# Kernel tuning notes

Measured on AMD Instinct MI355X. Metric: run time of the kernel, lower is better.

## Reference

```python
import jax, jax.numpy as jnp
import numpy as np
import math

B, S, HID = 2, 2048, 1024
NH = 16
HD = HID // NH          # 64
VD = HD // 2            # 32 value dim
TD = HD - VD            # 32 type dim
EPS = 1e-6


def setup_inputs() -> dict:
    key = jax.random.key(0)
    ks = jax.random.split(key, 12)
    std = 1.0 / math.sqrt(HID)
    xav = math.sqrt(6.0 / (TD + TD))
    return {
        "x": jax.random.normal(ks[0], (B, S, HID), dtype=jnp.float32),
        "q_w": jax.random.uniform(ks[1], (HID, HID), jnp.float32, -std, std),
        "q_b": jax.random.uniform(ks[2], (HID,), jnp.float32, -std, std),
        "k_w": jax.random.uniform(ks[3], (HID, HID), jnp.float32, -std, std),
        "k_b": jax.random.uniform(ks[4], (HID,), jnp.float32, -std, std),
        "v_w": jax.random.uniform(ks[5], (HID, HID), jnp.float32, -std, std),
        "v_b": jax.random.uniform(ks[6], (HID,), jnp.float32, -std, std),
        "out_w": jax.random.uniform(ks[7], (HID, HID), jnp.float32, -std, std),
        "out_b": jax.random.uniform(ks[8], (HID,), jnp.float32, -std, std),
        "type_bilinear": jax.random.uniform(ks[9], (NH, TD, TD), jnp.float32, -xav, xav),
        "type_bias": jnp.full((NH,), 2.0, dtype=jnp.float32),
        "mask": jnp.ones((B, S), dtype=jnp.int32),
    }


def reference(x, q_w, q_b, k_w, k_b, v_w, v_b, out_w, out_b, type_bilinear, type_bias, mask):
    # projections: [B,S,HID] -> [B,NH,S,HD]
    def proj(w, b):
        y = jnp.einsum("bsi,io->bso", x, w) + b
        return y.reshape(B, S, NH, HD).transpose(0, 2, 1, 3)

    q = proj(q_w, q_b)
    k = proj(k_w, k_b)
    v = proj(v_w, v_b)

    q_val, q_type = q[..., :VD], q[..., VD:]
    k_val, k_type = k[..., :VD], k[..., VD:]

    # standard value score: [B,NH,S,S]
    val_scores = jnp.einsum("bhqd,bhkd->bhqk", q_val, k_val) / math.sqrt(VD)

    # per-head bilinear type score: q_type @ W_h @ k_type^T + bias_h
    qt = jnp.einsum("bhqd,hde->bhqe", q_type, type_bilinear)
    type_scores = jnp.einsum("bhqe,bhke->bhqk", qt, k_type) + type_bias[None, :, None, None]
    type_unif = jax.nn.sigmoid(type_scores)

    scores = val_scores + jnp.log(type_unif + EPS)

    # mask: [B,S] -> broadcast over heads and query dim (keys masked)
    m = (mask[:, None, None, :] != 0)
    scores = jnp.where(m, scores, -jnp.inf)

    attn = jax.nn.softmax(scores, axis=-1)
    out = jnp.einsum("bhqk,bhkd->bhqd", attn, v)          # [B,NH,S,HD]
    out = out.transpose(0, 2, 1, 3).reshape(B, S, HID)
    return jnp.einsum("bsi,io->bso", out, out_w) + out_b
```

## Files before the change

kernel.cpp:

```cpp
#include <hip/hip_runtime.h>
#include <hip/hip_bf16.h>
#include <math.h>

typedef __attribute__((ext_vector_type(8))) short bf16x8;
typedef __attribute__((ext_vector_type(4))) short bf16x4;
typedef __attribute__((ext_vector_type(4))) float f32x4;
typedef __attribute__((ext_vector_type(4))) int   i32x4;

#define NHh 16
#define Sq  2048
#define HIDq 1024
#define HDq 64
#define LOG2E 1.4426950408889634f

#if __has_builtin(__builtin_amdgcn_exp2f)
#define EXP2F(x) __builtin_amdgcn_exp2f(x)
#else
#define EXP2F(x) exp2f(x)
#endif
#if __has_builtin(__builtin_amdgcn_rcpf)
#define RCPF(x) __builtin_amdgcn_rcpf(x)
#else
#define RCPF(x) (1.0f/(x))
#endif

#if __has_builtin(__builtin_amdgcn_mfma_f32_16x16x16bf16_1k)
__device__ __forceinline__ f32x4 MFMA16(bf16x4 a, bf16x4 b, f32x4 c){
  return __builtin_amdgcn_mfma_f32_16x16x16bf16_1k(a, b, c, 0, 0, 0);
}
#else
__device__ __forceinline__ f32x4 MFMA16(bf16x4 a, bf16x4 b, f32x4 c){
  asm volatile("v_mfma_f32_16x16x16_bf16 %0, %1, %2, %0\n\ts_nop 7\n\ts_nop 7"
               : "+v"(c) : "v"(a), "v"(b));
  return c;
}
#endif

__device__ __forceinline__ unsigned short f2bf(float f){
  union { float f; unsigned u; } v; v.f = f;
  unsigned r = v.u + 0x7fffu + ((v.u >> 16) & 1u);
  return (unsigned short)(r >> 16);
}
__device__ __forceinline__ float bf2f(unsigned short s){
  union { unsigned u; float f; } v; v.u = ((unsigned)s) << 16;
  return v.f;
}
__device__ __forceinline__ unsigned pk2bf(float lo, float hi){
  union { __hip_bfloat162 h; unsigned u; } w;
  w.h = __float22bfloat162_rn(make_float2(lo, hi));
  return w.u;
}

__device__ __forceinline__ void gload_lds16(const unsigned short* g, unsigned short* l){
  __builtin_amdgcn_global_load_lds(
      (const __attribute__((address_space(1))) unsigned int*)g,
      (__attribute__((address_space(3))) unsigned int*)l, 16, 0, 0);
}

__global__ __launch_bounds__(256) void convert_x(const float* __restrict__ in,
                                                 unsigned short* __restrict__ out, int n8,
                                                 const int* __restrict__ mask,
                                                 unsigned short* __restrict__ Mbf){
  int bid = blockIdx.x;
  int nmain = gridDim.x - 2;
  if (bid >= nmain){
    int base = (bid - nmain)*2048 + threadIdx.x*8;
    #pragma unroll
    for (int j=0;j<8;j++) Mbf[base+j] = mask[base+j] ? (unsigned short)0x3F80 : (unsigned short)0;
    return;
  }
  int i = bid*256 + threadIdx.x;
  if (i >= n8) return;
  const f32x4* p = (const f32x4*)(in + (size_t)i*8);
  f32x4 a = p[0], b = p[1];
  union { unsigned short us[8]; i32x4 v; } o;
  #pragma unroll
  for (int j=0;j<4;j++){ o.us[j] = f2bf(a[j]); o.us[4+j] = f2bf(b[j]); }
  *(i32x4*)(out + (size_t)i*8) = o.v;
}

__global__ __launch_bounds__(256) void transpose_w(const float* __restrict__ w0, const float* __restrict__ w1,
                                                   const float* __restrict__ w2, const float* __restrict__ w3,
                                                   unsigned short* __restrict__ wT){
  __shared__ float tile[32][33];
  int z = blockIdx.z;
  const float* w = (z==0)?w0:(z==1)?w1:(z==2)?w2:w3;
  unsigned short* dst = wT + (size_t)z*HIDq*HIDq;
  int tx = threadIdx.x, ty = threadIdx.y;
  int n0 = blockIdx.x*32, k0 = blockIdx.y*32;
  #pragma unroll
  for (int i=ty;i<32;i+=8) tile[i][tx] = w[(size_t)(k0+i)*HIDq + n0+tx];
  __syncthreads();
  #pragma unroll
  for (int i=ty;i<32;i+=8) dst[(size_t)(n0+i)*HIDq + k0+tx] = f2bf(tile[tx][i]);
}

__device__ __forceinline__ void gemm_core_gl(const unsigned short* __restrict__ Ag,
                                             const unsigned short* __restrict__ Bg,
                                             unsigned short* As, unsigned short* Bs,
                                             int t, int wv, int lane, int wr, int wc, int lr, int g,
                                             f32x4 acc[4][4]){
  for (int k0=0; k0<HIDq; k0+=64){
    __syncthreads();
    #pragma unroll
    for (int j=0;j<4;j++){
      int flat = (j*4+wv)*64 + lane;
      int row = flat>>3, c = flat&7;
      int srcc = (c ^ (row&7))*8;
      gload_lds16(Ag + (size_t)row*HIDq + k0 + srcc, &As[flat*8]);
      gload_lds16(Bg + (size_t)row*HIDq + k0 + srcc, &Bs[flat*8]);
    }
    __syncthreads();
    #pragma unroll
    for (int ks=0; ks<2; ks++){
      bf16x8 af[4], bfv[4];
      #pragma unroll
      for (int m=0;m<4;m++){
        int rr = wr + m*16 + lr;
        af[m]  = *(bf16x8*)&As[rr*64 + (((ks*4+g) ^ (rr&7))*8)];
      }
      #pragma unroll
      for (int n=0;n<4;n++){
        int rr = wc + n*16 + lr;
        bfv[n] = *(bf16x8*)&Bs[rr*64 + (((ks*4+g) ^ (rr&7))*8)];
      }
      #pragma unroll
      for (int n=0;n<4;n++)
        #pragma unroll
        for (int m=0;m<4;m++)
          acc[n][m] = __builtin_amdgcn_mfma_f32_16x16x32_bf16(bfv[n], af[m], acc[n][m], 0,0,0);
    }
  }
}

__global__ __launch_bounds__(256) void gemm_qkv(const unsigned short* __restrict__ xbf,
    const unsigned short* __restrict__ wT,
    const float* __restrict__ q_b, const float* __restrict__ k_b, const float* __restrict__ v_b,
    const int* __restrict__ mask,
    unsigned short* __restrict__ Qeff, unsigned short* __restrict__ Keff,
    unsigned short* __restrict__ Vt){
  __shared__ unsigned short As[128*64];
  __shared__ unsigned short Bs[128*64];
  const int t = threadIdx.x;
  const int wv = t>>6, lane = t&63, g = lane>>4, lr = lane&15;
  const int wr = (wv>>1)*64, wc = (wv&1)*64;
  f32x4 acc[4][4] = {};
  const int xb = blockIdx.x, yb = blockIdx.y;
  const float VS = 0.25501335f;

  if (xb < 16){
    const int row0 = yb*128, col0 = xb*128;
    gemm_core_gl(xbf + (size_t)row0*HIDq, wT + (size_t)col0*HIDq, As, Bs, t, wv, lane, wr, wc, lr, g, acc);
    #pragma unroll
    for (int n=0;n<4;n++){
      #pragma unroll
      for (int m=0;m<4;m++){
        int row = row0 + wr + m*16 + lr;
        int b_ = row>>11, ss = row&2047;
        int colb = col0 + wc + n*16 + g*4;
        int seg = colb>>10, cw = colb&1023;
        int hh = cw>>6, d = cw&63;
        const float* bp = seg ? k_b : q_b;
        f32x4 bb = *(const f32x4*)&bp[cw];
        float sc = seg ? 1.0f : (d < 32 ? VS : -LOG2E);
        unsigned short* E = seg ? Keff : Qeff;
        float v0 = (acc[n][m][0]+bb[0])*sc, v1 = (acc[n][m][1]+bb[1])*sc;
        float v2 = (acc[n][m][2]+bb[2])*sc, v3 = (acc[n][m][3]+bb[3])*sc;
        union { unsigned u[2]; unsigned long long ll; } W;
        W.u[0] = pk2bf(v0,v1); W.u[1] = pk2bf(v2,v3);
        *(unsigned long long*)&E[(((size_t)b_*NHh+hh)*Sq+ss)*HDq + d] = W.ll;
      }
    }
  } else {
    const int row0 = (xb-16)*128, col0 = yb*128;
    gemm_core_gl(wT + (size_t)2*HIDq*HIDq + (size_t)row0*HIDq, xbf + (size_t)col0*HIDq,
                 As, Bs, t, wv, lane, wr, wc, lr, g, acc);
    #pragma unroll
    for (int n=0;n<4;n++){
      #pragma unroll
      for (int m=0;m<4;m++){
        int chan = row0 + wr + m*16 + lr;
        int hh = chan>>6, d = chan&63;
        float bv = v_b[chan];
        int colb = col0 + wc + n*16 + g*4;
        int b_ = colb>>11, ss = colb&2047;
        i32x4 mk = *(const i32x4*)&mask[(size_t)b_*Sq + ss];
        float m0 = mk[0]?1.f:0.f, m1 = mk[1]?1.f:0.f, m2 = mk[2]?1.f:0.f, m3 = mk[3]?1.f:0.f;
        union { unsigned u[2]; unsigned long long ll; } W;
        W.u[0] = pk2bf((acc[n][m][0]+bv)*m0, (acc[n][m][1]+bv)*m1);
        W.u[1] = pk2bf((acc[n][m][2]+bv)*m2, (acc[n][m][3]+bv)*m3);
        *(unsigned long long*)&Vt[(((size_t)b_*NHh+hh)*HDq + d)*Sq + ss] = W.ll;
      }
    }
  }
}

__global__ __launch_bounds__(256) void gemm_out(const unsigned short* __restrict__ A,
                                                const unsigned short* __restrict__ Bt,
                                                const float* __restrict__ bias,
                                                float* __restrict__ C){
  __shared__ unsigned short As[128*64];
  __shared__ unsigned short Bs[64*64];
  const int t = threadIdx.x;
  const int wv = t>>6, lane = t&63, g = lane>>4, lr = lane&15;
  const int wr = (wv>>1)*64, wc = (wv&1)*32;
  const int row0 = blockIdx.y*128, col0 = blockIdx.x*64;
  f32x4 acc[2][4] = {};
  for (int k0=0; k0<HIDq; k0+=64){
    __syncthreads();
    #pragma unroll
    for (int j=0;j<4;j++){
      int flat = t + j*256;
      int row = flat>>3, c = flat&7;
      int srcc = (c ^ (row&7))*8;
      gload_lds16(A + (size_t)(row0+row)*HIDq + k0 + srcc, &As[flat*8]);
    }
    #pragma unroll
    for (int j=0;j<2;j++){
      int flat = t + j*256;
      int row = flat>>3, c = flat&7;
      int srcc = (c ^ (row&7))*8;
      gload_lds16(Bt + (size_t)(col0+row)*HIDq + k0 + srcc, &Bs[flat*8]);
    }
    __syncthreads();
    #pragma unroll
    for (int ks=0; ks<2; ks++){
      bf16x8 af[4], bfv[2];
      #pragma unroll
      for (int m=0;m<4;m++){
        int rr = wr + m*16 + lr;
        af[m]  = *(bf16x8*)&As[rr*64 + (((ks*4+g) ^ (rr&7))*8)];
      }
      #pragma unroll
      for (int n=0;n<2;n++){
        int rr = wc + n*16 + lr;
        bfv[n] = *(bf16x8*)&Bs[rr*64 + (((ks*4+g) ^ (rr&7))*8)];
      }
      #pragma unroll
      for (int n=0;n<2;n++)
        #pragma unroll
        for (int m=0;m<4;m++)
          acc[n][m] = __builtin_amdgcn_mfma_f32_16x16x32_bf16(bfv[n], af[m], acc[n][m], 0,0,0);
    }
  }
  #pragma unroll
  for (int n=0;n<2;n++){
    #pragma unroll
    for (int m=0;m<4;m++){
      int row = row0 + wr + m*16 + lr;
      int colb = col0 + wc + n*16 + g*4;
      f32x4 bb = *(const f32x4*)&bias[colb];
      f32x4 o = acc[n][m] + bb;
      *(f32x4*)&C[(size_t)row*HIDq + colb] = o;
    }
  }
}

__global__ __launch_bounds__(256,4) void attn_kernel(
    const unsigned short* __restrict__ Qe, const unsigned short* __restrict__ Ke,
    const unsigned short* __restrict__ Vt, const float* __restrict__ Tb,
    const float* __restrict__ tbias, const unsigned short* __restrict__ Mbf,
    unsigned short* __restrict__ Obuf)
{
  __shared__ __align__(16) unsigned char smem[40960];
  unsigned short* Kb0 = (unsigned short*)smem;
  unsigned short* Kb1 = (unsigned short*)(smem + 8192);
  unsigned short* Kb2 = (unsigned short*)(smem + 16384);
  unsigned short* Vb0 = (unsigned short*)(smem + 24576);
  unsigned short* Vb1 = (unsigned short*)(smem + 32768);
  float* qls = (float*)smem;
  unsigned short* qtls = Vb1;

  const int t = threadIdx.x;
  const int dd = blockIdx.x;
  const int slot = dd>>3, xcd = dd&7;
  const int x = slot & 31;
  const int bh = ((slot>>5)<<3) | xcd;
  const int h = bh & 15, b = bh >> 4;
  const int q0 = x*64;
  const int wv = t>>6, lane = t&63, g = lane>>4, lr = lane&15;

  const unsigned short* Qb  = Qe + (((size_t)b*NHh+h)*Sq + q0)*HDq;
  const unsigned short* Kb  = Ke + ((size_t)b*NHh+h)*(size_t)Sq*HDq;
  const unsigned short* Vtb = Vt + ((size_t)b*NHh+h)*(size_t)HDq*Sq;
  const unsigned short* Mbfb = Mbf + (size_t)b*Sq;

  {
    int row = t>>2, c8 = (t&3)*8;
    bf16x8 v = *(const bf16x8*)(Qb + (size_t)row*HDq + 32 + c8);
    #pragma unroll
    for (int j=0;j<8;j++) qls[row*33 + c8 + j] = bf2f((unsigned short)v[j]);
  }
  __syncthreads();
  {
    int row = t&63, e0 = (t>>6)*8;
    const float* Th = Tb + (size_t)h*1024;
    float a[8] = {};
    #pragma unroll 4
    for (int d=0; d<32; d++){
      float qd = qls[row*33 + d];
      const f32x4* tp = (const f32x4*)(Th + d*32 + e0);
      f32x4 t0 = tp[0], t1 = tp[1];
      a[0]+=qd*t0[0]; a[1]+=qd*t0[1]; a[2]+=qd*t0[2]; a[3]+=qd*t0[3];
      a[4]+=qd*t1[0]; a[5]+=qd*t1[1]; a[6]+=qd*t1[2]; a[7]+=qd*t1[3];
    }
    __syncthreads();
    union { unsigned u[2]; unsigned long long ll; } W0, W1;
    W0.u[0]=pk2bf(a[0],a[1]); W0.u[1]=pk2bf(a[2],a[3]);
    W1.u[0]=pk2bf(a[4],a[5]); W1.u[1]=pk2bf(a[6],a[7]);
    *(unsigned long long*)&qtls[row*40 + e0]     = W0.ll;
    *(unsigned long long*)&qtls[row*40 + e0 + 4] = W1.ll;
  }
  bf16x8 qvf = *(const bf16x8*)(Qb + (size_t)(wv*16+lr)*HDq + g*8);
  __syncthreads();
  bf16x8 qtn = *(const bf16x8*)&qtls[(wv*16+lr)*40 + g*8];
  __syncthreads();

  #pragma unroll
  for (int i=0;i<2;i++){
    int c = t + i*256;
    int kr = c>>3, kc = c&7;
    gload_lds16(Kb + (size_t)kr*HDq + ((kc ^ (kr&7))*8), Kb0 + c*8);
    int vd = c>>3, vc = c&7;
    gload_lds16(Vtb + (size_t)vd*Sq + ((vc ^ (vd&7))*8), Vb0 + c*8);
    gload_lds16(Kb + (size_t)(64+kr)*HDq + ((kc ^ (kr&7))*8), Kb1 + c*8);
  }
  __syncthreads();

  const float tbn = -tbias[h]*LOG2E;
  const f32x4 tbc = {tbn,tbn,tbn,tbn};
  const f32x4 zf = {0.f,0.f,0.f,0.f};
  f32x4 oT[4] = {};
  f32x4 lsum = {0.f,0.f,0.f,0.f};

  auto phase = [&](const unsigned short* Kc, const unsigned short* Vc, int key0,
                   bool stK, int keyK, unsigned short* Kn,
                   bool stV, int keyV, unsigned short* Vn, bool vm8){
    if (stK){
      #pragma unroll
      for (int i=0;i<2;i++){
        int c = t + i*256;
        int kr = c>>3, kc = c&7;
        gload_lds16(Kb + (size_t)(keyK+kr)*HDq + ((kc ^ (kr&7))*8), Kn + c*8);
      }
    }
    if (stV){
      #pragma unroll
      for (int i=0;i<2;i++){
        int c = t + i*256;
        int vd = c>>3, vc = c&7;
        gload_lds16(Vtb + (size_t)vd*Sq + keyV + ((vc ^ (vd&7))*8), Vn + c*8);
      }
    }
    if (vm8) asm volatile("s_waitcnt vmcnt(8)" ::: "memory");
    else     asm volatile("s_waitcnt vmcnt(4)" ::: "memory");
    __builtin_amdgcn_sched_barrier(0);
    __builtin_amdgcn_s_barrier();

    f32x4 sv[4], st[4];
    __builtin_amdgcn_s_setprio(1);
    #pragma unroll
    for (int ks=0; ks<4; ks++){
      const unsigned short* kb = Kc + (ks*16+lr)*64;
      bf16x8 kf0 = *(const bf16x8*)(kb + (((g  ) ^ (lr&7))*8));
      bf16x8 kf1 = *(const bf16x8*)(kb + (((4+g) ^ (lr&7))*8));
      sv[ks] = __builtin_amdgcn_mfma_f32_16x16x32_bf16(kf0, qvf, zf, 0,0,0);
      st[ks] = __builtin_amdgcn_mfma_f32_16x16x32_bf16(kf1, qtn, tbc, 0,0,0);
    }
    __builtin_amdgcn_s_setprio(0);
    bf16x4 pa[4];
    #pragma unroll
    for (int ks=0; ks<4; ks++){
      float p0 = EXP2F(sv[ks][0]) * RCPF(1.f + EXP2F(st[ks][0]));
      float p1 = EXP2F(sv[ks][1]) * RCPF(1.f + EXP2F(st[ks][1]));
      float p2 = EXP2F(sv[ks][2]) * RCPF(1.f + EXP2F(st[ks][2]));
      float p3 = EXP2F(sv[ks][3]) * RCPF(1.f + EXP2F(st[ks][3]));
      union { unsigned u[2]; bf16x4 v; } P_;
      P_.u[0] = pk2bf(p0,p1); P_.u[1] = pk2bf(p2,p3);
      pa[ks] = P_.v;
    }
    #pragma unroll
    for (int ks=0; ks<4; ks++){
      bf16x4 mfr = *(const bf16x4*)(Mbfb + key0 + ks*16 + g*4);
      __builtin_amdgcn_s_setprio(1);
      lsum = MFMA16(pa[ks], mfr, lsum);
      #pragma unroll
      for (int db=0; db<4; db++){
        bf16x4 vf = *(const bf16x4*)(Vc + (db*16+lr)*64 + (((2*ks + (g>>1)) ^ (lr&7))*8 + 4*(g&1)));
        oT[db] = MFMA16(pa[ks], vf, oT[db]);
      }
      __builtin_amdgcn_s_setprio(0);
    }
    __builtin_amdgcn_s_barrier();
  };

  for (int j=0; j<5; j++){
    int kt = j*384;
    phase(Kb0, Vb0, kt,      true, kt+128, Kb2,  true, kt+64,  Vb1, true);
    phase(Kb1, Vb1, kt+64,   true, kt+192, Kb0,  true, kt+128, Vb0, true);
    phase(Kb2, Vb0, kt+128,  true, kt+256, Kb1,  true, kt+192, Vb1, true);
    phase(Kb0, Vb1, kt+192,  true, kt+320, Kb2,  true, kt+256, Vb0, true);
    phase(Kb1, Vb0, kt+256,  true, kt+384, Kb0,  true, kt+320, Vb1, true);
    phase(Kb2, Vb1, kt+320,  (kt+448 < Sq), kt+448, Kb1,  true, kt+384, Vb0, true);
  }
  phase(Kb0, Vb0, 1920,  false, 0, Kb0,  true, 1984, Vb1, false);
  phase(Kb1, Vb1, 1984,  false, 0, Kb0,  false, 0, Vb0,  false);

  float linv[4];
  #pragma unroll
  for (int r=0;r<4;r++) linv[r] = (lsum[r] > 0.f) ? RCPF(lsum[r]) : 0.f;
  unsigned short* Ob = Obuf + ((size_t)b*Sq + (q0 + wv*16 + g*4))*HIDq + h*HDq + lr;
  #pragma unroll
  for (int db=0; db<4; db++){
    #pragma unroll
    for (int r=0;r<4;r++)
      Ob[(size_t)r*HIDq + db*16] = f2bf(oT[db][r]*linv[r]);
  }
}

extern "C" void kernel_launch(void* const* d_in, const int* in_sizes, int n_in,
                              void* d_out, int out_size, void* d_ws, size_t ws_size,
                              hipStream_t stream) {
  const float* x     = (const float*)d_in[0];
  const float* q_w   = (const float*)d_in[1];
  const float* q_b   = (const float*)d_in[2];
  const float* k_w   = (const float*)d_in[3];
  const float* k_b   = (const float*)d_in[4];
  const float* v_w   = (const float*)d_in[5];
  const float* v_b   = (const float*)d_in[6];
  const float* out_w = (const float*)d_in[7];
  const float* out_b = (const float*)d_in[8];
  const float* Tb    = (const float*)d_in[9];
  const float* tbias = (const float*)d_in[10];
  const int*   mask  = (const int*)d_in[11];

  const size_t MROWS = 4096;
  unsigned short* xbf  = (unsigned short*)d_ws;
  unsigned short* wT   = xbf  + MROWS*HIDq;
  unsigned short* Qeff = wT   + (size_t)4*HIDq*HIDq;
  unsigned short* Keff = Qeff + MROWS*HIDq;
  unsigned short* Vt   = Keff + MROWS*HIDq;
  unsigned short* Obuf = Vt   + MROWS*HIDq;
  unsigned short* Mbf  = Obuf + MROWS*HIDq;

  int n8 = (int)(MROWS*HIDq/8);
  convert_x<<<dim3(n8/256 + 2), dim3(256), 0, stream>>>(x, xbf, n8, mask, Mbf);
  transpose_w<<<dim3(32,32,4), dim3(32,8), 0, stream>>>(q_w, k_w, v_w, out_w, wT);

  gemm_qkv<<<dim3(24,32), dim3(256), 0, stream>>>(xbf, wT, q_b, k_b, v_b, mask, Qeff, Keff, Vt);

  attn_kernel<<<dim3(1024), dim3(256), 0, stream>>>(Qeff, Keff, Vt, Tb, tbias, Mbf, Obuf);

  gemm_out<<<dim3(16,32), dim3(256), 0, stream>>>(Obuf, wT + (size_t)3*HIDq*HIDq, out_b, (float*)d_out);
}
```

Measured before the change: 152.9 us.

## Double query tile per attention block and stage mask in LDS

Each attention workgroup now handles 128 queries instead of 64, with each wave processing two 16-row query fragments. Every K/V tile loaded into LDS is therefore reused across twice as many queries, and the grid is halved to 512 blocks. The K/V pipeline changes from an offset triple/double buffer to a simple double buffer that stages K and V together. The key mask is also preloaded into LDS instead of being read from global memory on each step. In exchange, register pressure roughly doubles (launch bounds drop to 2 waves per SIMD), and fewer blocks means less occupancy and less latency hiding.

```diff
diff --git a/kernel.cpp b/kernel.cpp
--- a/kernel.cpp
+++ b/kernel.cpp
@@ -256,28 +256,28 @@
   }
 }
 
-__global__ __launch_bounds__(256,4) void attn_kernel(
+__global__ __launch_bounds__(256,2) void attn_kernel(
     const unsigned short* __restrict__ Qe, const unsigned short* __restrict__ Ke,
     const unsigned short* __restrict__ Vt, const float* __restrict__ Tb,
     const float* __restrict__ tbias, const unsigned short* __restrict__ Mbf,
     unsigned short* __restrict__ Obuf)
 {
-  __shared__ __align__(16) unsigned char smem[40960];
+  __shared__ __align__(16) unsigned char smem[36864];
   unsigned short* Kb0 = (unsigned short*)smem;
   unsigned short* Kb1 = (unsigned short*)(smem + 8192);
-  unsigned short* Kb2 = (unsigned short*)(smem + 16384);
-  unsigned short* Vb0 = (unsigned short*)(smem + 24576);
-  unsigned short* Vb1 = (unsigned short*)(smem + 32768);
+  unsigned short* Vb0 = (unsigned short*)(smem + 16384);
+  unsigned short* Vb1 = (unsigned short*)(smem + 24576);
+  unsigned short* Msk = (unsigned short*)(smem + 32768);
   float* qls = (float*)smem;
-  unsigned short* qtls = Vb1;
+  unsigned short* qtls = (unsigned short*)(smem + 24576);
 
   const int t = threadIdx.x;
   const int dd = blockIdx.x;
   const int slot = dd>>3, xcd = dd&7;
-  const int x = slot & 31;
-  const int bh = ((slot>>5)<<3) | xcd;
+  const int x = slot & 15;
+  const int bh = ((slot>>4)<<3) | xcd;
   const int h = bh & 15, b = bh >> 4;
-  const int q0 = x*64;
+  const int q0 = x*128;
   const int wv = t>>6, lane = t&63, g = lane>>4, lr = lane&15;
 
   const unsigned short* Qb  = Qe + (((size_t)b*NHh+h)*Sq + q0)*HDq;
@@ -286,36 +286,45 @@
   const unsigned short* Mbfb = Mbf + (size_t)b*Sq;
 
   {
-    int row = t>>2, c8 = (t&3)*8;
-    bf16x8 v = *(const bf16x8*)(Qb + (size_t)row*HDq + 32 + c8);
-    #pragma unroll
-    for (int j=0;j<8;j++) qls[row*33 + c8 + j] = bf2f((unsigned short)v[j]);
+    int row = t>>1, c8 = (t&1)*16;
+    bf16x8 v0 = *(const bf16x8*)(Qb + (size_t)row*HDq + 32 + c8);
+    bf16x8 v1 = *(const bf16x8*)(Qb + (size_t)row*HDq + 32 + c8 + 8);
+    #pragma unroll
+    for (int j=0;j<8;j++){
+      qls[row*33 + c8 + j]     = bf2f((unsigned short)v0[j]);
+      qls[row*33 + c8 + 8 + j] = bf2f((unsigned short)v1[j]);
+    }
   }
   __syncthreads();
   {
-    int row = t&63, e0 = (t>>6)*8;
     const float* Th = Tb + (size_t)h*1024;
-    float a[8] = {};
-    #pragma unroll 4
-    for (int d=0; d<32; d++){
-      float qd = qls[row*33 + d];
-      const f32x4* tp = (const f32x4*)(Th + d*32 + e0);
-      f32x4 t0 = tp[0], t1 = tp[1];
-      a[0]+=qd*t0[0]; a[1]+=qd*t0[1]; a[2]+=qd*t0[2]; a[3]+=qd*t0[3];
-      a[4]+=qd*t1[0]; a[5]+=qd*t1[1]; a[6]+=qd*t1[2]; a[7]+=qd*t1[3];
-    }
-    __syncthreads();
-    union { unsigned u[2]; unsigned long long ll; } W0, W1;
-    W0.u[0]=pk2bf(a[0],a[1]); W0.u[1]=pk2bf(a[2],a[3]);
-    W1.u[0]=pk2bf(a[4],a[5]); W1.u[1]=pk2bf(a[6],a[7]);
-    *(unsigned long long*)&qtls[row*40 + e0]     = W0.ll;
-    *(unsigned long long*)&qtls[row*40 + e0 + 4] = W1.ll;
-  }
-  bf16x8 qvf = *(const bf16x8*)(Qb + (size_t)(wv*16+lr)*HDq + g*8);
+    #pragma unroll
+    for (int rp=0; rp<2; rp++){
+      int row = rp*64 + (t&63), e0 = (t>>6)*8;
+      float a[8] = {};
+      #pragma unroll 4
+      for (int d=0; d<32; d++){
+        float qd = qls[row*33 + d];
+        const f32x4* tp = (const f32x4*)(Th + d*32 + e0);
+        f32x4 t0 = tp[0], t1 = tp[1];
+        a[0]+=qd*t0[0]; a[1]+=qd*t0[1]; a[2]+=qd*t0[2]; a[3]+=qd*t0[3];
+        a[4]+=qd*t1[0]; a[5]+=qd*t1[1]; a[6]+=qd*t1[2]; a[7]+=qd*t1[3];
+      }
+      union { unsigned u[2]; unsigned long long ll; } W0, W1;
+      W0.u[0]=pk2bf(a[0],a[1]); W0.u[1]=pk2bf(a[2],a[3]);
+      W1.u[0]=pk2bf(a[4],a[5]); W1.u[1]=pk2bf(a[6],a[7]);
+      *(unsigned long long*)&qtls[row*40 + e0]     = W0.ll;
+      *(unsigned long long*)&qtls[row*40 + e0 + 4] = W1.ll;
+    }
+  }
+  bf16x8 qvf0 = *(const bf16x8*)(Qb + (size_t)(wv*32+lr)*HDq + g*8);
+  bf16x8 qvf1 = *(const bf16x8*)(Qb + (size_t)(wv*32+16+lr)*HDq + g*8);
   __syncthreads();
-  bf16x8 qtn = *(const bf16x8*)&qtls[(wv*16+lr)*40 + g*8];
+  bf16x8 qtn0 = *(const bf16x8*)&qtls[(wv*32+lr)*40 + g*8];
+  bf16x8 qtn1 = *(const bf16x8*)&qtls[(wv*32+16+lr)*40 + g*8];
   __syncthreads();
 
+  gload_lds16(Mbfb + t*8, Msk + t*8);
   #pragma unroll
   for (int i=0;i<2;i++){
     int c = t + i*256;
@@ -323,98 +332,111 @@
     gload_lds16(Kb + (size_t)kr*HDq + ((kc ^ (kr&7))*8), Kb0 + c*8);
     int vd = c>>3, vc = c&7;
     gload_lds16(Vtb + (size_t)vd*Sq + ((vc ^ (vd&7))*8), Vb0 + c*8);
-    gload_lds16(Kb + (size_t)(64+kr)*HDq + ((kc ^ (kr&7))*8), Kb1 + c*8);
   }
   __syncthreads();
 
   const float tbn = -tbias[h]*LOG2E;
   const f32x4 tbc = {tbn,tbn,tbn,tbn};
   const f32x4 zf = {0.f,0.f,0.f,0.f};
-  f32x4 oT[4] = {};
-  f32x4 lsum = {0.f,0.f,0.f,0.f};
+  f32x4 oT0[4] = {}, oT1[4] = {};
+  f32x4 lsum0 = {0.f,0.f,0.f,0.f}, lsum1 = {0.f,0.f,0.f,0.f};
 
   auto phase = [&](const unsigned short* Kc, const unsigned short* Vc, int key0,
-                   bool stK, int keyK, unsigned short* Kn,
-                   bool stV, int keyV, unsigned short* Vn, bool vm8){
-    if (stK){
+                   bool doStage, int keyN, unsigned short* Kn, unsigned short* Vn){
+    if (doStage){
       #pragma unroll
       for (int i=0;i<2;i++){
         int c = t + i*256;
         int kr = c>>3, kc = c&7;
-        gload_lds16(Kb + (size_t)(keyK+kr)*HDq + ((kc ^ (kr&7))*8), Kn + c*8);
-      }
-    }
-    if (stV){
-      #pragma unroll
-      for (int i=0;i<2;i++){
-        int c = t + i*256;
+        gload_lds16(Kb + (size_t)(keyN+kr)*HDq + ((kc ^ (kr&7))*8), Kn + c*8);
         int vd = c>>3, vc = c&7;
-        gload_lds16(Vtb + (size_t)vd*Sq + keyV + ((vc ^ (vd&7))*8), Vn + c*8);
-      }
-    }
-    if (vm8) asm volatile("s_waitcnt vmcnt(8)" ::: "memory");
-    else     asm volatile("s_waitcnt vmcnt(4)" ::: "memory");
+        gload_lds16(Vtb + (size_t)vd*Sq + keyN + ((vc ^ (vd&7))*8), Vn + c*8);
+      }
+      asm volatile("s_waitcnt vmcnt(4)" ::: "memory");
+    } else {
+      asm volatile("s_waitcnt vmcnt(0)" ::: "memory");
+    }
     __builtin_amdgcn_sched_barrier(0);
     __builtin_amdgcn_s_barrier();
 
-    f32x4 sv[4], st[4];
+    f32x4 sv0[4], st0[4], sv1[4], st1[4];
     __builtin_amdgcn_s_setprio(1);
     #pragma unroll
     for (int ks=0; ks<4; ks++){
       const unsigned short* kb = Kc + (ks*16+lr)*64;
       bf16x8 kf0 = *(const bf16x8*)(kb + (((g  ) ^ (lr&7))*8));
       bf16x8 kf1 = *(const bf16x8*)(kb + (((4+g) ^ (lr&7))*8));
-      sv[ks] = __builtin_amdgcn_mfma_f32_16x16x32_bf16(kf0, qvf, zf, 0,0,0);
-      st[ks] = __builtin_amdgcn_mfma_f32_16x16x32_bf16(kf1, qtn, tbc, 0,0,0);
+      sv0[ks] = __builtin_amdgcn_mfma_f32_16x16x32_bf16(kf0, qvf0, zf, 0,0,0);
+      st0[ks] = __builtin_amdgcn_mfma_f32_16x16x32_bf16(kf1, qtn0, tbc, 0,0,0);
+      sv1[ks] = __builtin_amdgcn_mfma_f32_16x16x32_bf16(kf0, qvf1, zf, 0,0,0);
+      st1[ks] = __builtin_amdgcn_mfma_f32_16x16x32_bf16(kf1, qtn1, tbc, 0,0,0);
     }
     __builtin_amdgcn_s_setprio(0);
-    bf16x4 pa[4];
+    bf16x4 pa0[4], pa1[4];
     #pragma unroll
     for (int ks=0; ks<4; ks++){
-      float p0 = EXP2F(sv[ks][0]) * RCPF(1.f + EXP2F(st[ks][0]));
-      float p1 = EXP2F(sv[ks][1]) * RCPF(1.f + EXP2F(st[ks][1]));
-      float p2 = EXP2F(sv[ks][2]) * RCPF(1.f + EXP2F(st[ks][2]));
-      float p3 = EXP2F(sv[ks][3]) * RCPF(1.f + EXP2F(st[ks][3]));
-      union { unsigned u[2]; bf16x4 v; } P_;
-      P_.u[0] = pk2bf(p0,p1); P_.u[1] = pk2bf(p2,p3);
-      pa[ks] = P_.v;
+      {
+        float p0 = EXP2F(sv0[ks][0]) * RCPF(1.f + EXP2F(st0[ks][0]));
+        float p1 = EXP2F(sv0[ks][1]) * RCPF(1.f + EXP2F(st0[ks][1]));
+        float p2 = EXP2F(sv0[ks][2]) * RCPF(1.f + EXP2F(st0[ks][2]));
+        float p3 = EXP2F(sv0[ks][3]) * RCPF(1.f + EXP2F(st0[ks][3]));
+        union { unsigned u[2]; bf16x4 v; } P_;
+        P_.u[0] = pk2bf(p0,p1); P_.u[1] = pk2bf(p2,p3);
+        pa0[ks] = P_.v;
+      }
+      {
+        float p0 = EXP2F(sv1[ks][0]) * RCPF(1.f + EXP2F(st1[ks][0]));
+        float p1 = EXP2F(sv1[ks][1]) * RCPF(1.f + EXP2F(st1[ks][1]));
+        float p2 = EXP2F(sv1[ks][2]) * RCPF(1.f + EXP2F(st1[ks][2]));
+        float p3 = EXP2F(sv1[ks][3]) * RCPF(1.f + EXP2F(st1[ks][3]));
+        union { unsigned u[2]; bf16x4 v; } P_;
+        P_.u[0] = pk2bf(p0,p1); P_.u[1] = pk2bf(p2,p3);
+        pa1[ks] = P_.v;
+      }
     }
     #pragma unroll
     for (int ks=0; ks<4; ks++){
-      bf16x4 mfr = *(const bf16x4*)(Mbfb + key0 + ks*16 + g*4);
+      bf16x4 mfr = *(const bf16x4*)(Msk + key0 + ks*16 + g*4);
       __builtin_amdgcn_s_setprio(1);
-      lsum = MFMA16(pa[ks], mfr, lsum);
+      lsum0 = MFMA16(pa0[ks], mfr, lsum0);
+      lsum1 = MFMA16(pa1[ks], mfr, lsum1);
       #pragma unroll
       for (int db=0; db<4; db++){
         bf16x4 vf = *(const bf16x4*)(Vc + (db*16+lr)*64 + (((2*ks + (g>>1)) ^ (lr&7))*8 + 4*(g&1)));
-        oT[db] = MFMA16(pa[ks], vf, oT[db]);
+        oT0[db] = MFMA16(pa0[ks], vf, oT0[db]);
+        oT1[db] = MFMA16(pa1[ks], vf, oT1[db]);
       }
       __builtin_amdgcn_s_setprio(0);
     }
     __builtin_amdgcn_s_barrier();
   };
 
-  for (int j=0; j<5; j++){
-    int kt = j*384;
-    phase(Kb0, Vb0, kt,      true, kt+128, Kb2,  true, kt+64,  Vb1, true);
-    phase(Kb1, Vb1, kt+64,   true, kt+192, Kb0,  true, kt+128, Vb0, true);
-    phase(Kb2, Vb0, kt+128,  true, kt+256, Kb1,  true, kt+192, Vb1, true);
-    phase(Kb0, Vb1, kt+192,  true, kt+320, Kb2,  true, kt+256, Vb0, true);
-    phase(Kb1, Vb0, kt+256,  true, kt+384, Kb0,  true, kt+320, Vb1, true);
-    phase(Kb2, Vb1, kt+320,  (kt+448 < Sq), kt+448, Kb1,  true, kt+384, Vb0, true);
-  }
-  phase(Kb0, Vb0, 1920,  false, 0, Kb0,  true, 1984, Vb1, false);
-  phase(Kb1, Vb1, 1984,  false, 0, Kb0,  false, 0, Vb0,  false);
-
-  float linv[4];
-  #pragma unroll
-  for (int r=0;r<4;r++) linv[r] = (lsum[r] > 0.f) ? RCPF(lsum[r]) : 0.f;
-  unsigned short* Ob = Obuf + ((size_t)b*Sq + (q0 + wv*16 + g*4))*HIDq + h*HDq + lr;
-  #pragma unroll
-  for (int db=0; db<4; db++){
-    #pragma unroll
-    for (int r=0;r<4;r++)
-      Ob[(size_t)r*HIDq + db*16] = f2bf(oT[db][r]*linv[r]);
+  for (int kt=0; kt<Sq; kt+=128){
+    phase(Kb0, Vb0, kt,      true,           kt+64,  Kb1, Vb1);
+    phase(Kb1, Vb1, kt+64,   kt+128 < Sq,    kt+128, Kb0, Vb0);
+  }
+
+  float linv0[4], linv1[4];
+  #pragma unroll
+  for (int r=0;r<4;r++){
+    linv0[r] = (lsum0[r] > 0.f) ? RCPF(lsum0[r]) : 0.f;
+    linv1[r] = (lsum1[r] > 0.f) ? RCPF(lsum1[r]) : 0.f;
+  }
+  {
+    unsigned short* Ob = Obuf + ((size_t)b*Sq + (q0 + wv*32 + g*4))*HIDq + h*HDq + lr;
+    #pragma unroll
+    for (int db=0; db<4; db++)
+      #pragma unroll
+      for (int r=0;r<4;r++)
+        Ob[(size_t)r*HIDq + db*16] = f2bf(oT0[db][r]*linv0[r]);
+  }
+  {
+    unsigned short* Ob = Obuf + ((size_t)b*Sq + (q0 + wv*32 + 16 + g*4))*HIDq + h*HDq + lr;
+    #pragma unroll
+    for (int db=0; db<4; db++)
+      #pragma unroll
+      for (int r=0;r<4;r++)
+        Ob[(size_t)r*HIDq + db*16] = f2bf(oT1[db][r]*linv1[r]);
   }
 }
 
@@ -449,7 +471,7 @@
 
   gemm_qkv<<<dim3(24,32), dim3(256), 0, stream>>>(xbf, wT, q_b, k_b, v_b, mask, Qeff, Keff, Vt);
 
-  attn_kernel<<<dim3(1024), dim3(256), 0, stream>>>(Qeff, Keff, Vt, Tb, tbias, Mbf, Obuf);
+  attn_kernel<<<dim3(512), dim3(256), 0, stream>>>(Qeff, Keff, Vt, Tb, tbias, Mbf, Obuf);
 
   gemm_out<<<dim3(16,32), dim3(256), 0, stream>>>(Obuf, wT + (size_t)3*HIDq*HIDq, out_b, (float*)d_out);
 }
```

Result: no change. 154.3 us (+1.0%).
